# Performance work log

Hardware: AMD Instinct MI355X
Metric: run time of the kernel (lower is better)

Reference implementation:

```python
import jax, jax.numpy as jnp
import numpy as np

B, A, D, REL, H = 8, 192, 128, 5, 128

def setup_inputs() -> dict:
    key = jax.random.key(0)
    ks = jax.random.split(key, 10)
    coord = jax.random.normal(ks[0], (B, A, D), jnp.float32)
    goal = jax.random.normal(ks[1], (B, A, D), jnp.float32)
    frontier = jax.random.normal(ks[2], (B, A, D), jnp.float32)
    rel_feat = jax.random.normal(ks[3], (B, A, A, REL), jnp.float32)
    rule_adj = jax.random.randint(ks[4], (B, A, A), 0, 2) > 0
    base_score = jax.random.normal(ks[5], (B, A, A), jnp.float32)
    graph_context = jax.random.normal(ks[6], (B, D), jnp.float32)
    fan_in = 6 * D + REL + D
    W1 = jax.random.normal(ks[7], (fan_in, H), jnp.float32) / np.sqrt(fan_in)
    b1 = jnp.zeros((H,), jnp.float32)
    W2 = jax.random.normal(ks[8], (H, 1), jnp.float32) / np.sqrt(H)
    b2 = jnp.zeros((1,), jnp.float32)
    return {"coord": coord, "goal": goal, "frontier": frontier, "rel_feat": rel_feat,
            "rule_adj": rule_adj, "base_score": base_score, "graph_context": graph_context,
            "W1": W1, "b1": b1, "W2": W2, "b2": b2}

def reference(coord, goal, frontier, rel_feat, rule_adj, base_score, graph_context, W1, b1, W2, b2):
    b, a, d = coord.shape
    def pair(x):
        xi = jnp.broadcast_to(x[:, :, None, :], (b, a, a, d))
        xj = jnp.broadcast_to(x[:, None, :, :], (b, a, a, d))
        return xi, xj
    ci, cj = pair(coord)
    gi, gj = pair(goal)
    fi, fj = pair(frontier)
    gc = jnp.broadcast_to(graph_context[:, None, None, :], (b, a, a, d))
    edge_in = jnp.concatenate([ci, cj, gi, gj, fi, fj, rel_feat, gc], axis=-1)  # [B,A,A,7D+rel]
    h = jax.nn.relu(edge_in @ W1 + b1)
    learned = (h @ W2 + b2)[..., 0]  # [B,A,A]
    score = base_score + learned
    score = jnp.where(rule_adj, score, jnp.float32(-1e9))
    weights = jax.nn.softmax(score, axis=-1)
    weights = weights * rule_adj.astype(weights.dtype)
    weights = weights / (weights.sum(axis=-1, keepdims=True) + 1e-8)
    return weights, score, learned
```

## Files before the change

### kernel.cpp

```cpp
#include <hip/hip_runtime.h>
#include <math.h>

#define NB 8
#define NA 192
#define ND 128
#define NREL 5
#define NH 128
#define ROWS 6
#define KS 4
#define NROWBLK ((NB * NA) / ROWS)
#define TI 2

__global__ __launch_bounds__(256, 4) void precompute_P(
    const float* __restrict__ coord, const float* __restrict__ goal,
    const float* __restrict__ frontier, const float* __restrict__ gctx,
    const float* __restrict__ W1, const float* __restrict__ b1,
    float* __restrict__ PiP, float* __restrict__ PjTP, float* __restrict__ Gc)
{
    const int blk = blockIdx.x;
    const int tid = threadIdx.x;

    if (blk >= KS * NROWBLK) {
        __shared__ float red[256];
        const int b = blk - KS * NROWBLK;
        const int h = tid & 127, part = tid >> 7;
        const float* g = gctx + b * ND + part * 64;
        const float* w = W1 + (size_t)(6 * ND + NREL + part * 64) * NH + h;
        float acc = 0.f;
#pragma unroll 8
        for (int d = 0; d < 64; ++d) acc += g[d] * w[d * NH];
        red[tid] = acc;
        __syncthreads();
        if (part == 0) Gc[b * NH + h] = red[h] + red[h + 128] + b1[h];
        return;
    }

    const int rb = blk >> 2;
    const int kq = blk & 3;
    const int r0 = rb * ROWS;

    __shared__ __align__(16) float X[ROWS][96];

    for (int idx = tid; idx < ROWS * 96; idx += 256) {
        int r = idx / 96;
        int kk = idx - r * 96;
        int k = kq * 96 + kk;
        int s = k >> 7, d = k & 127;
        const float* src = (s == 0) ? coord : (s == 1) ? goal : frontier;
        X[r][kk] = src[(r0 + r) * ND + d];
    }
    __syncthreads();

    const int colLocal = tid & 127;
    const int role = tid >> 7;
    const int roleOff = role * 128;

    float acc[ROWS];
#pragma unroll
    for (int r = 0; r < ROWS; r++) acc[r] = 0.f;

    auto seg = [&](int kkStart, int sChunk, int dStart, int len) {
        const float* wb = W1 + (size_t)(sChunk * 256 + roleOff + dStart) * NH + colLocal;
#pragma unroll 4
        for (int t = 0; t < len; t += 4) {
            float w0 = wb[0 * NH];
            float w1 = wb[1 * NH];
            float w2 = wb[2 * NH];
            float w3 = wb[3 * NH];
            wb += 4 * NH;
#pragma unroll
            for (int r = 0; r < ROWS; r++) {
                float4 x = *(const float4*)&X[r][kkStart + t];
                acc[r] += x.x * w0 + x.y * w1 + x.z * w2 + x.w * w3;
            }
        }
    };
    if (kq == 0)      { seg(0, 0, 0, 96); }
    else if (kq == 1) { seg(0, 0, 96, 32); seg(32, 1, 0, 64); }
    else if (kq == 2) { seg(0, 1, 64, 64); seg(64, 2, 0, 32); }
    else              { seg(0, 2, 32, 96); }

#pragma unroll
    for (int r = 0; r < ROWS; r++) {
        int row = r0 + r;
        if (role == 0) {
            PiP[((size_t)kq * NB * NA + row) * NH + colLocal] = acc[r];
        } else {
            int b = row / NA, a = row - b * NA;
            PjTP[(((size_t)kq * NB + b) * NH + colLocal) * NA + a] = acc[r];
        }
    }
}

__global__ __launch_bounds__(256) void combine_PjT(
    const float* __restrict__ PjTP, float* __restrict__ PjT)
{
    const size_t e = (size_t)blockIdx.x * 256 + threadIdx.x;
    const size_t n = (size_t)NB * NH * NA;
    float v = PjTP[e] + PjTP[n + e] + PjTP[2 * n + e] + PjTP[3 * n + e];
    PjT[e] = v;
}

__global__ __launch_bounds__(384, 4) void edge_kernel(
    const float* __restrict__ PiP, const float* __restrict__ PjT,
    const float* __restrict__ Gc, const float* __restrict__ W1,
    const float* __restrict__ W2, const float* __restrict__ b2v,
    const float* __restrict__ rel_feat, const int* __restrict__ rule_adj,
    const float* __restrict__ base_score,
    float* __restrict__ out_w, float* __restrict__ out_s, float* __restrict__ out_l)
{
    const int b  = blockIdx.x / (NA / TI);
    const int i0 = (blockIdx.x % (NA / TI)) * TI;
    const int tid = threadIdx.x;
    const int j = tid % NA;
    const int half = tid / NA;

    __shared__ __align__(16) float4 su1[NH];
    __shared__ __align__(16) float4 su2[NH];
    __shared__ float s_part[2][TI][NA];
    __shared__ float redA[3], redB[3], redC[3];

    if (tid < NH) {
        const int h = tid;
        const int row0 = b * NA + i0;
        float pig0 = Gc[b * NH + h], pig1 = pig0;
#pragma unroll
        for (int kq = 0; kq < KS; ++kq) {
            pig0 += PiP[((size_t)kq * NB * NA + row0) * NH + h];
            pig1 += PiP[((size_t)kq * NB * NA + row0 + 1) * NH + h];
        }
        const float* wr = W1 + (size_t)(6 * ND) * NH + h;
        su1[h] = make_float4(wr[0 * NH], wr[1 * NH], wr[2 * NH], wr[3 * NH]);
        su2[h] = make_float4(wr[4 * NH], W2[h], pig0, pig1);
    }

    float r0v[NREL], r1v[NREL];
    {
        const float* rf0 = rel_feat + (((size_t)(b * NA + i0) * NA) + j) * NREL;
        const float* rf1 = rf0 + (size_t)NA * NREL;
#pragma unroll
        for (int r = 0; r < NREL; r++) { r0v[r] = rf0[r]; r1v[r] = rf1[r]; }
    }
    __syncthreads();

    const float* pjb = PjT + ((size_t)b * NH + half * 64) * NA + j;
    float acc0 = 0.f, acc1 = 0.f;
#pragma unroll 4
    for (int hh = 0; hh < 64; ++hh) {
        float p = pjb[hh * NA];
        float4 a = su1[half * 64 + hh];
        float4 c = su2[half * 64 + hh];
        float pre0 = c.z + p;
        pre0 += r0v[0] * a.x; pre0 += r0v[1] * a.y; pre0 += r0v[2] * a.z;
        pre0 += r0v[3] * a.w; pre0 += r0v[4] * c.x;
        float pre1 = c.w + p;
        pre1 += r1v[0] * a.x; pre1 += r1v[1] * a.y; pre1 += r1v[2] * a.z;
        pre1 += r1v[3] * a.w; pre1 += r1v[4] * c.x;
        acc0 += fmaxf(pre0, 0.f) * c.y;
        acc1 += fmaxf(pre1, 0.f) * c.y;
    }
    s_part[half][0][j] = acc0;
    s_part[half][1][j] = acc1;
    __syncthreads();

    const int wave = tid >> 6, lane = tid & 63;
    const float b2c = b2v[0];
    float scv[TI];
    int adjv[TI];
    if (tid < NA) {
#pragma unroll
        for (int ti = 0; ti < TI; ++ti) {
            const size_t row = (size_t)(b * NA + i0 + ti) * NA + tid;
            float lrn = s_part[0][ti][tid] + s_part[1][ti][tid] + b2c;
            out_l[row] = lrn;
            adjv[ti] = rule_adj[row];
            scv[ti] = adjv[ti] ? (base_score[row] + lrn) : -1e9f;
            out_s[row] = scv[ti];
        }
    }

#pragma unroll
    for (int ti = 0; ti < TI; ++ti) {
        float m = (tid < NA) ? scv[ti] : -3.4e38f;
#pragma unroll
        for (int off = 32; off > 0; off >>= 1) m = fmaxf(m, __shfl_xor(m, off, 64));
        if (lane == 0 && wave < 3) redA[wave] = m;
        __syncthreads();
        m = fmaxf(fmaxf(redA[0], redA[1]), redA[2]);

        float e = (tid < NA) ? __expf(scv[ti] - m) : 0.f;
        float S = e;
#pragma unroll
        for (int off = 32; off > 0; off >>= 1) S += __shfl_xor(S, off, 64);
        if (lane == 0 && wave < 3) redB[wave] = S;
        __syncthreads();
        S = redB[0] + redB[1] + redB[2];

        float wj = (tid < NA && adjv[ti]) ? e * (1.f / S) : 0.f;
        float sw = wj;
#pragma unroll
        for (int off = 32; off > 0; off >>= 1) sw += __shfl_xor(sw, off, 64);
        if (lane == 0 && wave < 3) redC[wave] = sw;
        __syncthreads();
        sw = redC[0] + redC[1] + redC[2];

        if (tid < NA)
            out_w[(size_t)(b * NA + i0 + ti) * NA + tid] = wj * (1.f / (sw + 1e-8f));
        __syncthreads();
    }
}

extern "C" void kernel_launch(void* const* d_in, const int* in_sizes, int n_in,
                              void* d_out, int out_size, void* d_ws, size_t ws_size,
                              hipStream_t stream) {
    const float* coord    = (const float*)d_in[0];
    const float* goal     = (const float*)d_in[1];
    const float* frontier = (const float*)d_in[2];
    const float* rel_feat = (const float*)d_in[3];
    const int*   rule_adj = (const int*)d_in[4];
    const float* base_sc  = (const float*)d_in[5];
    const float* gctx     = (const float*)d_in[6];
    const float* W1       = (const float*)d_in[7];
    const float* b1       = (const float*)d_in[8];
    const float* W2       = (const float*)d_in[9];
    const float* b2       = (const float*)d_in[10];

    float* PiP  = (float*)d_ws;
    float* PjTP = PiP + KS * NB * NA * NH;
    float* PjT  = PjTP + KS * NB * NH * NA;
    float* Gc   = PjT + NB * NH * NA;

    float* out_w = (float*)d_out;
    float* out_s = out_w + NB * NA * NA;
    float* out_l = out_s + NB * NA * NA;

    precompute_P<<<KS * NROWBLK + NB, 256, 0, stream>>>(coord, goal, frontier, gctx,
                                                        W1, b1, PiP, PjTP, Gc);
    combine_PjT<<<(NB * NH * NA) / 256, 256, 0, stream>>>(PjTP, PjT);
    edge_kernel<<<NB * (NA / TI), 384, 0, stream>>>(PiP, PjT, Gc, W1, W2, b2, rel_feat,
                                                    rule_adj, base_sc, out_w, out_s, out_l);
}
```

Before: 118.8 us.

## Split precompute K into halves and fold partial-sum combine into edge kernel

The precompute kernel now splits the 384-long K dimension into two halves instead of four and processes 3 rows per block rather than 6. The separate combine_PjT launch goes away, and the edge kernel sums the two PjT partials inline while reading them. This cuts one kernel launch and a full read/write pass of the partial buffer. In exchange, the edge kernel's inner loop now does two global loads per iteration, and the precompute blocks each do more serial K work.

```diff
diff --git a/kernel.cpp b/kernel.cpp
--- a/kernel.cpp
+++ b/kernel.cpp
@@ -6,8 +6,7 @@
 #define ND 128
 #define NREL 5
 #define NH 128
-#define ROWS 6
-#define KS 4
+#define ROWS 3
 #define NROWBLK ((NB * NA) / ROWS)
 #define TI 2
 
@@ -20,9 +19,9 @@
     const int blk = blockIdx.x;
     const int tid = threadIdx.x;
 
-    if (blk >= KS * NROWBLK) {
+    if (blk >= 2 * NROWBLK) {
         __shared__ float red[256];
-        const int b = blk - KS * NROWBLK;
+        const int b = blk - 2 * NROWBLK;
         const int h = tid & 127, part = tid >> 7;
         const float* g = gctx + b * ND + part * 64;
         const float* w = W1 + (size_t)(6 * ND + NREL + part * 64) * NH + h;
@@ -35,16 +34,16 @@
         return;
     }
 
-    const int rb = blk >> 2;
-    const int kq = blk & 3;
+    const int rb = blk >> 1;
+    const int kh = blk & 1;
     const int r0 = rb * ROWS;
 
-    __shared__ __align__(16) float X[ROWS][96];
-
-    for (int idx = tid; idx < ROWS * 96; idx += 256) {
-        int r = idx / 96;
-        int kk = idx - r * 96;
-        int k = kq * 96 + kk;
+    __shared__ __align__(16) float X[ROWS][192];
+
+    for (int idx = tid; idx < ROWS * 192; idx += 256) {
+        int r = idx / 192;
+        int kk = idx - r * 192;
+        int k = kh * 192 + kk;
         int s = k >> 7, d = k & 127;
         const float* src = (s == 0) ? coord : (s == 1) ? goal : frontier;
         X[r][kk] = src[(r0 + r) * ND + d];
@@ -75,34 +74,23 @@
             }
         }
     };
-    if (kq == 0)      { seg(0, 0, 0, 96); }
-    else if (kq == 1) { seg(0, 0, 96, 32); seg(32, 1, 0, 64); }
-    else if (kq == 2) { seg(0, 1, 64, 64); seg(64, 2, 0, 32); }
-    else              { seg(0, 2, 32, 96); }
+    if (kh == 0) { seg(0, 0, 0, 128); seg(128, 1, 0, 64); }
+    else         { seg(0, 1, 64, 64); seg(64, 2, 0, 128); }
 
 #pragma unroll
     for (int r = 0; r < ROWS; r++) {
         int row = r0 + r;
         if (role == 0) {
-            PiP[((size_t)kq * NB * NA + row) * NH + colLocal] = acc[r];
+            PiP[((size_t)kh * NB * NA + row) * NH + colLocal] = acc[r];
         } else {
             int b = row / NA, a = row - b * NA;
-            PjTP[(((size_t)kq * NB + b) * NH + colLocal) * NA + a] = acc[r];
+            PjTP[(((size_t)kh * NB + b) * NH + colLocal) * NA + a] = acc[r];
         }
     }
 }
 
-__global__ __launch_bounds__(256) void combine_PjT(
-    const float* __restrict__ PjTP, float* __restrict__ PjT)
-{
-    const size_t e = (size_t)blockIdx.x * 256 + threadIdx.x;
-    const size_t n = (size_t)NB * NH * NA;
-    float v = PjTP[e] + PjTP[n + e] + PjTP[2 * n + e] + PjTP[3 * n + e];
-    PjT[e] = v;
-}
-
 __global__ __launch_bounds__(384, 4) void edge_kernel(
-    const float* __restrict__ PiP, const float* __restrict__ PjT,
+    const float* __restrict__ PiP, const float* __restrict__ PjTP,
     const float* __restrict__ Gc, const float* __restrict__ W1,
     const float* __restrict__ W2, const float* __restrict__ b2v,
     const float* __restrict__ rel_feat, const int* __restrict__ rule_adj,
@@ -123,12 +111,12 @@
     if (tid < NH) {
         const int h = tid;
         const int row0 = b * NA + i0;
-        float pig0 = Gc[b * NH + h], pig1 = pig0;
-#pragma unroll
-        for (int kq = 0; kq < KS; ++kq) {
-            pig0 += PiP[((size_t)kq * NB * NA + row0) * NH + h];
-            pig1 += PiP[((size_t)kq * NB * NA + row0 + 1) * NH + h];
-        }
+        float pig0 = Gc[b * NH + h]
+                   + PiP[(size_t)row0 * NH + h]
+                   + PiP[(size_t)(NB * NA + row0) * NH + h];
+        float pig1 = Gc[b * NH + h]
+                   + PiP[(size_t)(row0 + 1) * NH + h]
+                   + PiP[(size_t)(NB * NA + row0 + 1) * NH + h];
         const float* wr = W1 + (size_t)(6 * ND) * NH + h;
         su1[h] = make_float4(wr[0 * NH], wr[1 * NH], wr[2 * NH], wr[3 * NH]);
         su2[h] = make_float4(wr[4 * NH], W2[h], pig0, pig1);
@@ -143,11 +131,12 @@
     }
     __syncthreads();
 
-    const float* pjb = PjT + ((size_t)b * NH + half * 64) * NA + j;
+    const float* pjb0 = PjTP + ((size_t)b * NH + half * 64) * NA + j;
+    const float* pjb1 = pjb0 + (size_t)NB * NH * NA;
     float acc0 = 0.f, acc1 = 0.f;
 #pragma unroll 4
     for (int hh = 0; hh < 64; ++hh) {
-        float p = pjb[hh * NA];
+        float p = pjb0[hh * NA] + pjb1[hh * NA];
         float4 a = su1[half * 64 + hh];
         float4 c = su2[half * 64 + hh];
         float pre0 = c.z + p;
@@ -226,17 +215,15 @@
     const float* b2       = (const float*)d_in[10];
 
     float* PiP  = (float*)d_ws;
-    float* PjTP = PiP + KS * NB * NA * NH;
-    float* PjT  = PjTP + KS * NB * NH * NA;
-    float* Gc   = PjT + NB * NH * NA;
+    float* PjTP = PiP + 2 * NB * NA * NH;
+    float* Gc   = PjTP + 2 * NB * NH * NA;
 
     float* out_w = (float*)d_out;
     float* out_s = out_w + NB * NA * NA;
     float* out_l = out_s + NB * NA * NA;
 
-    precompute_P<<<KS * NROWBLK + NB, 256, 0, stream>>>(coord, goal, frontier, gctx,
-                                                        W1, b1, PiP, PjTP, Gc);
-    combine_PjT<<<(NB * NH * NA) / 256, 256, 0, stream>>>(PjTP, PjT);
-    edge_kernel<<<NB * (NA / TI), 384, 0, stream>>>(PiP, PjT, Gc, W1, W2, b2, rel_feat,
+    precompute_P<<<2 * NROWBLK + NB, 256, 0, stream>>>(coord, goal, frontier, gctx,
+                                                       W1, b1, PiP, PjTP, Gc);
+    edge_kernel<<<NB * (NA / TI), 384, 0, stream>>>(PiP, PjTP, Gc, W1, W2, b2, rel_feat,
                                                     rule_adj, base_sc, out_w, out_s, out_l);
 }
```

After: 112.6 us, median of 2. 5.2% less time.
